# Kernel tuning notes

Hardware: AMD Instinct MI355X
Metric: run time of the kernel (lower is better)

The kernel has to match this reference:

```python
import jax, jax.numpy as jnp
import numpy as np
import math

D_MODEL = 2048
R = 512
N_HEADS = 16
D_K = R // N_HEADS  # 32
B = 2
S = 2048


def _xavier(key, out_dim, in_dim):
    limit = math.sqrt(6.0 / (in_dim + out_dim))
    return jax.random.uniform(key, (out_dim, in_dim), jnp.float32, -limit, limit)


def setup_inputs() -> dict:
    key = jax.random.key(0)
    ks = jax.random.split(key, 6)
    x = jax.random.normal(ks[0], (B, S, D_MODEL), dtype=jnp.float32)
    mask = jnp.ones((B, 1, 1, S), dtype=jnp.int32)
    # torch nn.Linear weights have shape (out, in)
    Wq = _xavier(ks[1], R, D_MODEL)
    Wk = _xavier(ks[2], R, D_MODEL)
    Wv = _xavier(ks[3], R, D_MODEL)
    Wo = _xavier(ks[4], D_MODEL, R)
    bq = jnp.zeros((R,), jnp.float32)
    bk = jnp.zeros((R,), jnp.float32)
    bv = jnp.zeros((R,), jnp.float32)
    bo = jnp.zeros((D_MODEL,), jnp.float32)
    return {"x": x, "Wq": Wq, "bq": bq, "Wk": Wk, "bk": bk,
            "Wv": Wv, "bv": bv, "Wo": Wo, "bo": bo, "mask": mask}


def reference(x, Wq, bq, Wk, bk, Wv, bv, Wo, bo, mask):
    b, s, _ = x.shape
    scale = math.sqrt(D_K)
    # projections: (B,S,d_model) @ (d_model,r) -> (B,S,r)
    Q = x @ Wq.T + bq
    K = x @ Wk.T + bk
    V = x @ Wv.T + bv
    # (B,S,r) -> (B,H,S,d_k)
    Q = Q.reshape(b, s, N_HEADS, D_K).transpose(0, 2, 1, 3)
    K = K.reshape(b, s, N_HEADS, D_K).transpose(0, 2, 1, 3)
    V = V.reshape(b, s, N_HEADS, D_K).transpose(0, 2, 1, 3)
    # scores: (B,H,Sq,Sk)
    scores = jnp.einsum('bhqd,bhkd->bhqk', Q, K) / scale
    scores = jnp.where(mask == 0, -jnp.inf, scores)
    attn = jax.nn.softmax(scores, axis=-1)  # dropout p=0 (eval)
    out = jnp.einsum('bhqk,bhkd->bhqd', attn, V)
    out = out.transpose(0, 2, 1, 3).reshape(b, s, R)
    return out @ Wo.T + bo
```

## Files before the change

### kernel.cpp

```cpp
#include <hip/hip_runtime.h>
#include <hip/hip_bf16.h>
#include <math.h>

typedef __attribute__((ext_vector_type(8))) short bf16x8;
typedef __attribute__((ext_vector_type(4))) float f32x4;

#define D_MODEL 2048
#define R_DIM 512
#define N_HEADS 16
#define D_K 32
#define B_SZ 2
#define SEQ 2048
#define M_ROWS (B_SZ * SEQ)
#define N_QKV 1536
#define QSCALE 0.2550627231338903f
#define PS_STRIDE 68

__device__ __forceinline__ void dma16(const void* g, void* l)
{
    __builtin_amdgcn_global_load_lds(
        (const __attribute__((address_space(1))) void*)g,
        (__attribute__((address_space(3))) void*)l, 16, 0, 0);
}

__global__ __launch_bounds__(256) void cvt_inputs(
    const float* __restrict__ x,  __hip_bfloat16* __restrict__ xb,
    const float* __restrict__ Wq, const float* __restrict__ Wk,
    const float* __restrict__ Wv, const float* __restrict__ Wo,
    __hip_bfloat16* __restrict__ Wqkvb, __hip_bfloat16* __restrict__ Wob,
    const float* __restrict__ bq, const float* __restrict__ bk,
    const float* __restrict__ bv, float* __restrict__ bias_qkv,
    const int* __restrict__ mask, float* __restrict__ mbias)
{
    const int by = blockIdx.y;
    const int tid = blockIdx.x * blockDim.x + threadIdx.x;
    const int nthr = gridDim.x * blockDim.x;
    if (by == 5) {
        for (int i = tid; i < N_QKV; i += nthr) {
            float v = (i < 512) ? bq[i] * QSCALE
                    : (i < 1024) ? bk[i - 512] : bv[i - 1024];
            bias_qkv[i] = v;
        }
        for (int i = tid; i < B_SZ * SEQ; i += nthr)
            mbias[i] = mask[i] ? 0.0f : -1e30f;
        return;
    }
    const float* src; __hip_bfloat16* dst; float sc = 1.0f; int n;
    switch (by) {
      case 0: src = Wq; dst = Wqkvb; sc = QSCALE; n = R_DIM * D_MODEL; break;
      case 1: src = Wk; dst = Wqkvb + (size_t)R_DIM * D_MODEL; n = R_DIM * D_MODEL; break;
      case 2: src = Wv; dst = Wqkvb + (size_t)2 * R_DIM * D_MODEL; n = R_DIM * D_MODEL; break;
      case 3: src = Wo; dst = Wob; n = D_MODEL * R_DIM; break;
      default: src = x;  dst = xb;  n = M_ROWS * D_MODEL; break;
    }
    const int n4 = n >> 2;
    for (int i = tid; i < n4; i += nthr) {
        float4 f = ((const float4*)src)[i];
        union { ushort4 u; __hip_bfloat16 h[4]; } r;
        r.h[0] = __float2bfloat16(f.x * sc); r.h[1] = __float2bfloat16(f.y * sc);
        r.h[2] = __float2bfloat16(f.z * sc); r.h[3] = __float2bfloat16(f.w * sc);
        ((ushort4*)dst)[i] = r.u;
    }
}

template<bool OUT_BF16>
__global__ __launch_bounds__(256, 4) void gemm_dma(
    const __hip_bfloat16* __restrict__ A,
    const __hip_bfloat16* __restrict__ W,
    const float* __restrict__ bias,
    void* __restrict__ Cv,
    int N, int K)
{
    __shared__ __hip_bfloat16 As[128 * 64];
    __shared__ __hip_bfloat16 Bs[64 * 64];

    const int tid = threadIdx.x, lane = tid & 63, w = tid >> 6;
    const int l15 = lane & 15, q = lane >> 4;
    const int bm = blockIdx.y * 128, bn = blockIdx.x * 64;
    const int m_off = (w & 1) * 64, n_off = (w >> 1) * 32;

    const int lrow = lane >> 3;
    const int lc   = (lane & 7) ^ lrow;

    f32x4 acc[4][2] = {};

    for (int kt = 0; kt < K; kt += 64) {
        if (kt) __syncthreads();
        #pragma unroll
        for (int j = 0; j < 4; j++) {
            int row = (w * 4 + j) * 8 + lrow;
            dma16(&A[(size_t)(bm + row) * K + kt + lc * 8], &As[(w * 4 + j) * 512]);
        }
        #pragma unroll
        for (int j = 0; j < 2; j++) {
            int row = (w * 2 + j) * 8 + lrow;
            dma16(&W[(size_t)(bn + row) * K + kt + lc * 8], &Bs[(w * 2 + j) * 512]);
        }
        __syncthreads();

        #pragma unroll
        for (int ks = 0; ks < 2; ks++) {
            bf16x8 af[4], bf[2];
            #pragma unroll
            for (int t = 0; t < 4; t++) {
                int row = m_off + t * 16 + l15;
                af[t] = *(const bf16x8*)&As[row * 64 + (((ks * 4 + q) ^ (l15 & 7)) * 8)];
            }
            #pragma unroll
            for (int u = 0; u < 2; u++) {
                int row = n_off + u * 16 + l15;
                bf[u] = *(const bf16x8*)&Bs[row * 64 + (((ks * 4 + q) ^ (l15 & 7)) * 8)];
            }
            #pragma unroll
            for (int mt = 0; mt < 4; mt++)
                #pragma unroll
                for (int nt = 0; nt < 2; nt++)
                    acc[mt][nt] = __builtin_amdgcn_mfma_f32_16x16x32_bf16(
                        af[mt], bf[nt], acc[mt][nt], 0, 0, 0);
        }
    }

    #pragma unroll
    for (int mt = 0; mt < 4; mt++) {
        #pragma unroll
        for (int nt = 0; nt < 2; nt++) {
            int gm = bm + m_off + mt * 16 + q * 4;
            int gn = bn + n_off + nt * 16 + l15;
            float bv = bias[gn];
            #pragma unroll
            for (int r = 0; r < 4; r++) {
                float v = acc[mt][nt][r] + bv;
                if (OUT_BF16)
                    ((__hip_bfloat16*)Cv)[(size_t)(gm + r) * N + gn] = __float2bfloat16(v);
                else
                    ((float*)Cv)[(size_t)(gm + r) * N + gn] = v;
            }
        }
    }
}

__global__ __launch_bounds__(256) void flash_attn3(
    const __hip_bfloat16* __restrict__ QKV,
    const float* __restrict__ mbias,
    __hip_bfloat16* __restrict__ O)
{
    __shared__ __hip_bfloat16 Ks[64 * 40];
    __shared__ __hip_bfloat16 Vt[32 * 72];
    __shared__ __hip_bfloat16 Ps[4][16 * PS_STRIDE];

    const int tid = threadIdx.x, lane = tid & 63, w = tid >> 6;
    const int l15 = lane & 15, q = lane >> 4;
    const int qt = blockIdx.x & 31;
    const int h = (blockIdx.x >> 5) & 15;
    const int b = blockIdx.x >> 9;
    const int q0 = qt * 64;

    const int qrow = q0 + w * 16 + l15;
    bf16x8 qa = *(const bf16x8*)&QKV[(size_t)(b * SEQ + qrow) * N_QKV + h * D_K + q * 8];

    f32x4 oacc[2] = {};
    float rsum[4] = {0.f, 0.f, 0.f, 0.f};

    const int kv_k = tid >> 2, d0_k = (tid & 3) * 8;
    const int kv_v = tid & 63, d0_v = (tid >> 6) * 8;

    const __hip_bfloat16* Kp = QKV + R_DIM + h * D_K;
    const __hip_bfloat16* Vp = QKV + 2 * R_DIM + h * D_K;

    uint4 kreg = *(const uint4*)&Kp[(size_t)(b * SEQ + kv_k) * N_QKV + d0_k];
    uint4 vreg = *(const uint4*)&Vp[(size_t)(b * SEQ + kv_v) * N_QKV + d0_v];
    float mreg[4];
    #pragma unroll
    for (int nt = 0; nt < 4; nt++) mreg[nt] = mbias[b * SEQ + nt * 16 + l15];

    for (int kt = 0; kt < SEQ; kt += 64) {
        if (kt) __syncthreads();
        *(uint4*)&Ks[kv_k * 40 + d0_k] = kreg;
        union { uint4 u; __hip_bfloat16 hv[8]; } vv; vv.u = vreg;
        #pragma unroll
        for (int j = 0; j < 8; j++)
            Vt[(d0_v + j) * 72 + kv_v] = vv.hv[j];
        __syncthreads();

        float mv[4];
        #pragma unroll
        for (int nt = 0; nt < 4; nt++) mv[nt] = mreg[nt];
        if (kt + 64 < SEQ) {
            kreg = *(const uint4*)&Kp[(size_t)(b * SEQ + kt + 64 + kv_k) * N_QKV + d0_k];
            vreg = *(const uint4*)&Vp[(size_t)(b * SEQ + kt + 64 + kv_v) * N_QKV + d0_v];
            #pragma unroll
            for (int nt = 0; nt < 4; nt++)
                mreg[nt] = mbias[b * SEQ + kt + 64 + nt * 16 + l15];
        }

        f32x4 sc[4];
        #pragma unroll
        for (int nt = 0; nt < 4; nt++) {
            bf16x8 kb = *(const bf16x8*)&Ks[(nt * 16 + l15) * 40 + q * 8];
            f32x4 z = {};
            sc[nt] = __builtin_amdgcn_mfma_f32_16x16x32_bf16(qa, kb, z, 0, 0, 0);
        }
        #pragma unroll
        for (int nt = 0; nt < 4; nt++) {
            #pragma unroll
            for (int r = 0; r < 4; r++) {
                float p = __builtin_amdgcn_exp2f(sc[nt][r] + mv[nt]);
                rsum[r] += p;
                Ps[w][(q * 4 + r) * PS_STRIDE + nt * 16 + l15] = __float2bfloat16(p);
            }
        }
        #pragma unroll
        for (int ks = 0; ks < 2; ks++) {
            union { bf16x8 v; ushort4 h[2]; } pu;
            pu.h[0] = *(const ushort4*)&Ps[w][l15 * PS_STRIDE + ks * 32 + q * 8];
            pu.h[1] = *(const ushort4*)&Ps[w][l15 * PS_STRIDE + ks * 32 + q * 8 + 4];
            #pragma unroll
            for (int dt = 0; dt < 2; dt++) {
                bf16x8 vb = *(const bf16x8*)&Vt[(dt * 16 + l15) * 72 + ks * 32 + q * 8];
                oacc[dt] = __builtin_amdgcn_mfma_f32_16x16x32_bf16(pu.v, vb, oacc[dt], 0, 0, 0);
            }
        }
    }

    #pragma unroll
    for (int r = 0; r < 4; r++) {
        float s = rsum[r];
        #pragma unroll
        for (int off = 8; off >= 1; off >>= 1)
            s += __shfl_xor(s, off, 64);
        rsum[r] = s;
    }
    #pragma unroll
    for (int r = 0; r < 4; r++) {
        float inv = 1.0f / rsum[r];
        int row = q0 + w * 16 + q * 4 + r;
        #pragma unroll
        for (int dt = 0; dt < 2; dt++) {
            O[(size_t)(b * SEQ + row) * R_DIM + h * D_K + dt * 16 + l15] =
                __float2bfloat16(oacc[dt][r] * inv);
        }
    }
}

extern "C" void kernel_launch(void* const* d_in, const int* in_sizes, int n_in,
                              void* d_out, int out_size, void* d_ws, size_t ws_size,
                              hipStream_t stream)
{
    const float* x  = (const float*)d_in[0];
    const float* Wq = (const float*)d_in[1];
    const float* bq = (const float*)d_in[2];
    const float* Wk = (const float*)d_in[3];
    const float* bk = (const float*)d_in[4];
    const float* Wv = (const float*)d_in[5];
    const float* bv = (const float*)d_in[6];
    const float* Wo = (const float*)d_in[7];
    const float* bo = (const float*)d_in[8];
    const int* mask = (const int*)d_in[9];
    float* out = (float*)d_out;

    char* p = (char*)d_ws;
    __hip_bfloat16* xb     = (__hip_bfloat16*)p;
    __hip_bfloat16* AO     = xb;
    __hip_bfloat16* Wqkvb  = (__hip_bfloat16*)(p + (16u << 20));
    __hip_bfloat16* Wob    = (__hip_bfloat16*)(p + (22u << 20));
    float*          biasq  = (float*)(p + (24u << 20));
    float*          mbias  = (float*)(p + (24u << 20) + 8192);
    __hip_bfloat16* QKVb   = (__hip_bfloat16*)(p + (25u << 20));

    dim3 blk(256);
    hipLaunchKernelGGL(cvt_inputs, dim3(96, 6), blk, 0, stream,
                       x, xb, Wq, Wk, Wv, Wo, Wqkvb, Wob, bq, bk, bv, biasq, mask, mbias);
    hipLaunchKernelGGL((gemm_dma<true>), dim3(N_QKV / 64, M_ROWS / 128), blk, 0, stream,
                       xb, Wqkvb, biasq, QKVb, N_QKV, D_MODEL);
    hipLaunchKernelGGL(flash_attn3, dim3(B_SZ * N_HEADS * (SEQ / 64)), blk, 0, stream,
                       QKVb, mbias, AO);
    hipLaunchKernelGGL((gemm_dma<false>), dim3(D_MODEL / 64, M_ROWS / 128), blk, 0, stream,
                       AO, Wob, bo, out, D_MODEL, R_DIM);
}
```

Baseline: 231.8 us.

## Keep attention probabilities in registers via transposed QK^T and double-buffered V

The score MFMA is computed as K·Qᵀ, so each lane holds probabilities already in the layout the P·V MFMA needs as its A operand. This removes the per-wave Ps shared-memory round trip, and K fragments now load straight from global into registers instead of going through LDS. V is double-buffered in LDS, which allows one barrier per tile instead of two. Blocks are also swizzled across groups of eight, probabilities are packed to bf16 with v_cvt_pk_bf16_f32, and launch bounds request 4 blocks per CU. The trade-offs are more vector registers for the double-buffered K/V fragments, uncoalesced row-wise K loads from global, and a shuffle-based row-sum reduction at the end.

```diff
diff --git a/kernel.cpp b/kernel.cpp
--- a/kernel.cpp
+++ b/kernel.cpp
@@ -14,13 +14,19 @@
 #define M_ROWS (B_SZ * SEQ)
 #define N_QKV 1536
 #define QSCALE 0.2550627231338903f
-#define PS_STRIDE 68
 
 __device__ __forceinline__ void dma16(const void* g, void* l)
 {
     __builtin_amdgcn_global_load_lds(
         (const __attribute__((address_space(1))) void*)g,
         (__attribute__((address_space(3))) void*)l, 16, 0, 0);
+}
+
+__device__ __forceinline__ unsigned cvt_pk_bf16(float lo, float hi)
+{
+    unsigned r;
+    asm("v_cvt_pk_bf16_f32 %0, %1, %2" : "=v"(r) : "v"(lo), "v"(hi));
+    return r;
 }
 
 __global__ __launch_bounds__(256) void cvt_inputs(
@@ -139,101 +145,116 @@
     }
 }
 
-__global__ __launch_bounds__(256) void flash_attn3(
+__global__ __launch_bounds__(256, 4) void flash_attn4(
     const __hip_bfloat16* __restrict__ QKV,
     const float* __restrict__ mbias,
     __hip_bfloat16* __restrict__ O)
 {
-    __shared__ __hip_bfloat16 Ks[64 * 40];
-    __shared__ __hip_bfloat16 Vt[32 * 72];
-    __shared__ __hip_bfloat16 Ps[4][16 * PS_STRIDE];
+    __shared__ __hip_bfloat16 Vt[2][32 * 72];
 
     const int tid = threadIdx.x, lane = tid & 63, w = tid >> 6;
-    const int l15 = lane & 15, q = lane >> 4;
-    const int qt = blockIdx.x & 31;
-    const int h = (blockIdx.x >> 5) & 15;
-    const int b = blockIdx.x >> 9;
+    const int l15 = lane & 15, qg = lane >> 4;
+
+    const int nwg = (int)gridDim.x;
+    const int swz = (blockIdx.x & 7) * (nwg >> 3) + (blockIdx.x >> 3);
+    const int qt = swz & 31;
+    const int h  = (swz >> 5) & 15;
+    const int b  = swz >> 9;
     const int q0 = qt * 64;
 
-    const int qrow = q0 + w * 16 + l15;
-    bf16x8 qa = *(const bf16x8*)&QKV[(size_t)(b * SEQ + qrow) * N_QKV + h * D_K + q * 8];
+    const bf16x8 qa = *(const bf16x8*)
+        &QKV[(size_t)(b * SEQ + q0 + w * 16 + l15) * N_QKV + h * D_K + qg * 8];
+
+    const int kv_v = tid & 63, d0_v = (tid >> 6) * 8;
+    const __hip_bfloat16* Kp = QKV + (size_t)b * SEQ * N_QKV + R_DIM + h * D_K;
+    const __hip_bfloat16* Vp = QKV + (size_t)b * SEQ * N_QKV + 2 * R_DIM + h * D_K;
+    const float* mb_base = mbias + b * SEQ;
 
     f32x4 oacc[2] = {};
-    float rsum[4] = {0.f, 0.f, 0.f, 0.f};
-
-    const int kv_k = tid >> 2, d0_k = (tid & 3) * 8;
-    const int kv_v = tid & 63, d0_v = (tid >> 6) * 8;
-
-    const __hip_bfloat16* Kp = QKV + R_DIM + h * D_K;
-    const __hip_bfloat16* Vp = QKV + 2 * R_DIM + h * D_K;
-
-    uint4 kreg = *(const uint4*)&Kp[(size_t)(b * SEQ + kv_k) * N_QKV + d0_k];
-    uint4 vreg = *(const uint4*)&Vp[(size_t)(b * SEQ + kv_v) * N_QKV + d0_v];
-    float mreg[4];
+    float rsum = 0.f;
+
+    bf16x8 kfA[4], kfB[4];
+    uint4 vregA, vregB;
+
     #pragma unroll
-    for (int nt = 0; nt < 4; nt++) mreg[nt] = mbias[b * SEQ + nt * 16 + l15];
-
-    for (int kt = 0; kt < SEQ; kt += 64) {
-        if (kt) __syncthreads();
-        *(uint4*)&Ks[kv_k * 40 + d0_k] = kreg;
-        union { uint4 u; __hip_bfloat16 hv[8]; } vv; vv.u = vreg;
-        #pragma unroll
-        for (int j = 0; j < 8; j++)
-            Vt[(d0_v + j) * 72 + kv_v] = vv.hv[j];
-        __syncthreads();
-
-        float mv[4];
-        #pragma unroll
-        for (int nt = 0; nt < 4; nt++) mv[nt] = mreg[nt];
-        if (kt + 64 < SEQ) {
-            kreg = *(const uint4*)&Kp[(size_t)(b * SEQ + kt + 64 + kv_k) * N_QKV + d0_k];
-            vreg = *(const uint4*)&Vp[(size_t)(b * SEQ + kt + 64 + kv_v) * N_QKV + d0_v];
-            #pragma unroll
-            for (int nt = 0; nt < 4; nt++)
-                mreg[nt] = mbias[b * SEQ + kt + 64 + nt * 16 + l15];
-        }
-
-        f32x4 sc[4];
-        #pragma unroll
-        for (int nt = 0; nt < 4; nt++) {
-            bf16x8 kb = *(const bf16x8*)&Ks[(nt * 16 + l15) * 40 + q * 8];
-            f32x4 z = {};
-            sc[nt] = __builtin_amdgcn_mfma_f32_16x16x32_bf16(qa, kb, z, 0, 0, 0);
-        }
-        #pragma unroll
-        for (int nt = 0; nt < 4; nt++) {
-            #pragma unroll
-            for (int r = 0; r < 4; r++) {
-                float p = __builtin_amdgcn_exp2f(sc[nt][r] + mv[nt]);
-                rsum[r] += p;
-                Ps[w][(q * 4 + r) * PS_STRIDE + nt * 16 + l15] = __float2bfloat16(p);
-            }
-        }
-        #pragma unroll
-        for (int ks = 0; ks < 2; ks++) {
-            union { bf16x8 v; ushort4 h[2]; } pu;
-            pu.h[0] = *(const ushort4*)&Ps[w][l15 * PS_STRIDE + ks * 32 + q * 8];
-            pu.h[1] = *(const ushort4*)&Ps[w][l15 * PS_STRIDE + ks * 32 + q * 8 + 4];
-            #pragma unroll
-            for (int dt = 0; dt < 2; dt++) {
-                bf16x8 vb = *(const bf16x8*)&Vt[(dt * 16 + l15) * 72 + ks * 32 + q * 8];
-                oacc[dt] = __builtin_amdgcn_mfma_f32_16x16x32_bf16(pu.v, vb, oacc[dt], 0, 0, 0);
-            }
-        }
-    }
+    for (int nt = 0; nt < 4; nt++)
+        kfA[nt] = *(const bf16x8*)&Kp[(size_t)(nt * 16 + l15) * N_QKV + qg * 8];
+    vregA = *(const uint4*)&Vp[(size_t)kv_v * N_QKV + d0_v];
+
+#define FA_EXP(SC, MB, PA, U0, U1)                                              \
+    {                                                                           \
+        float p0 = __builtin_amdgcn_exp2f(SC[0] + MB.x);                        \
+        float p1 = __builtin_amdgcn_exp2f(SC[1] + MB.y);                        \
+        float p2 = __builtin_amdgcn_exp2f(SC[2] + MB.z);                        \
+        float p3 = __builtin_amdgcn_exp2f(SC[3] + MB.w);                        \
+        rsum += (p0 + p1) + (p2 + p3);                                          \
+        PA.u[U0] = cvt_pk_bf16(p0, p1);                                         \
+        PA.u[U1] = cvt_pk_bf16(p2, p3);                                         \
+    }
+
+#define FA_ITER(KT, BUF, KF, VREG, KFN, VREGN)                                  \
+    {                                                                           \
+                           \
+        union { uint4 u; __hip_bfloat16 hv[8]; } vv; vv.u = VREG;               \
+        _Pragma("unroll")                                                       \
+        for (int j = 0; j < 8; j++)                                             \
+            Vt[BUF][(d0_v + j) * 72 + kv_v] = vv.hv[j];                         \
+                     \
+        float4 mb0 = *(const float4*)&mb_base[(KT) +  0 + qg * 4];              \
+        float4 mb1 = *(const float4*)&mb_base[(KT) + 16 + qg * 4];              \
+        float4 mb2 = *(const float4*)&mb_base[(KT) + 32 + qg * 4];              \
+        float4 mb3 = *(const float4*)&mb_base[(KT) + 48 + qg * 4];              \
+                                     \
+        if ((KT) + 64 < SEQ) {                                                  \
+            _Pragma("unroll")                                                   \
+            for (int nt = 0; nt < 4; nt++)                                      \
+                KFN[nt] = *(const bf16x8*)                                      \
+                    &Kp[(size_t)((KT) + 64 + nt * 16 + l15) * N_QKV + qg * 8];  \
+            VREGN = *(const uint4*)&Vp[(size_t)((KT) + 64 + kv_v) * N_QKV + d0_v]; \
+        }                                                                       \
+           \
+        f32x4 sc0, sc1, sc2, sc3;                                               \
+        { f32x4 z = {}; sc0 = __builtin_amdgcn_mfma_f32_16x16x32_bf16(KF[0], qa, z, 0, 0, 0); } \
+        { f32x4 z = {}; sc1 = __builtin_amdgcn_mfma_f32_16x16x32_bf16(KF[1], qa, z, 0, 0, 0); } \
+        { f32x4 z = {}; sc2 = __builtin_amdgcn_mfma_f32_16x16x32_bf16(KF[2], qa, z, 0, 0, 0); } \
+        { f32x4 z = {}; sc3 = __builtin_amdgcn_mfma_f32_16x16x32_bf16(KF[3], qa, z, 0, 0, 0); } \
+              \
+        union { unsigned u[4]; bf16x8 v; } pa0, pa1;                            \
+        FA_EXP(sc0, mb0, pa0, 0, 1)                                             \
+        FA_EXP(sc1, mb1, pa0, 2, 3)                                             \
+        FA_EXP(sc2, mb2, pa1, 0, 1)                                             \
+        FA_EXP(sc3, mb3, pa1, 2, 3)                                             \
+        __syncthreads();            \
+         \
+        _Pragma("unroll")                                                       \
+        for (int dt = 0; dt < 2; dt++) {                                        \
+            const __hip_bfloat16* vrow = &Vt[BUF][(dt * 16 + l15) * 72];        \
+            union { unsigned u[4]; bf16x8 v; } vb0, vb1;                        \
+            *(uint2*)&vb0.u[0] = *(const uint2*)&vrow[     qg * 4];             \
+            *(uint2*)&vb0.u[2] = *(const uint2*)&vrow[16 + qg * 4];             \
+            *(uint2*)&vb1.u[0] = *(const uint2*)&vrow[32 + qg * 4];             \
+            *(uint2*)&vb1.u[2] = *(const uint2*)&vrow[48 + qg * 4];             \
+            oacc[dt] = __builtin_amdgcn_mfma_f32_16x16x32_bf16(pa0.v, vb0.v, oacc[dt], 0, 0, 0); \
+            oacc[dt] = __builtin_amdgcn_mfma_f32_16x16x32_bf16(pa1.v, vb1.v, oacc[dt], 0, 0, 0); \
+        }                                                                       \
+    }
+
+    for (int kt = 0; kt < SEQ; kt += 128) {
+        FA_ITER(kt,      0, kfA, vregA, kfB, vregB)
+        FA_ITER(kt + 64, 1, kfB, vregB, kfA, vregA)
+    }
+#undef FA_ITER
+#undef FA_EXP
+
+    float s = rsum;
+    s += __shfl_xor(s, 16, 64);
+    s += __shfl_xor(s, 32, 64);
 
     #pragma unroll
     for (int r = 0; r < 4; r++) {
-        float s = rsum[r];
-        #pragma unroll
-        for (int off = 8; off >= 1; off >>= 1)
-            s += __shfl_xor(s, off, 64);
-        rsum[r] = s;
-    }
-    #pragma unroll
-    for (int r = 0; r < 4; r++) {
-        float inv = 1.0f / rsum[r];
-        int row = q0 + w * 16 + q * 4 + r;
+        float rs = __shfl(s, qg * 4 + r, 64);
+        float inv = 1.0f / rs;
+        int row = q0 + w * 16 + qg * 4 + r;
         #pragma unroll
         for (int dt = 0; dt < 2; dt++) {
             O[(size_t)(b * SEQ + row) * R_DIM + h * D_K + dt * 16 + l15] =
@@ -272,7 +293,7 @@
                        x, xb, Wq, Wk, Wv, Wo, Wqkvb, Wob, bq, bk, bv, biasq, mask, mbias);
     hipLaunchKernelGGL((gemm_dma<true>), dim3(N_QKV / 64, M_ROWS / 128), blk, 0, stream,
                        xb, Wqkvb, biasq, QKVb, N_QKV, D_MODEL);
-    hipLaunchKernelGGL(flash_attn3, dim3(B_SZ * N_HEADS * (SEQ / 64)), blk, 0, stream,
+    hipLaunchKernelGGL(flash_attn4, dim3(B_SZ * N_HEADS * (SEQ / 64)), blk, 0, stream,
                        QKVb, mbias, AO);
     hipLaunchKernelGGL((gemm_dma<false>), dim3(D_MODEL / 64, M_ROWS / 128), blk, 0, stream,
                        AO, Wob, bo, out, D_MODEL, R_DIM);
```

After: 268.2 us. 15.7% more time.
